# Performance work log

Hardware: AMD Instinct MI355X
Metric: run time of the kernel (lower is better)

Reference implementation:

```python
import jax, jax.numpy as jnp
import numpy as np

H, HEADS, LAYERS = 512, 4, 3
HD = H // HEADS
FFN = 4 * H
B, S = 4, 2048
EPS = 1e-5
SCALE_BASE = 512.0
GAMMAS = (1.0 - np.exp(np.linspace(np.log(1.0 / 32.0), np.log(1.0 / 512.0), HEADS))).astype(np.float32)


def _xpos(x, downscale):
    # x: [B, heads, L, d]; standard XPOS rotary with per-dim decay scale
    L, d = x.shape[-2], x.shape[-1]
    half = d // 2
    s = (jnp.arange(half, dtype=jnp.float32) + 0.4 * d) / (1.4 * d)          # [half]
    pos = jnp.arange(L, dtype=jnp.float32)
    scale = s[None, :] ** (pos[:, None] / SCALE_BASE)                         # [L, half]
    inv_freq = 1.0 / (10000.0 ** (jnp.arange(half, dtype=jnp.float32) / half))
    ang = pos[:, None] * inv_freq[None, :]                                    # [L, half]
    if downscale:
        scale = 1.0 / scale
    sin_s = jnp.repeat(jnp.sin(ang) * scale, 2, axis=-1)                      # [L, d]
    cos_s = jnp.repeat(jnp.cos(ang) * scale, 2, axis=-1)
    x1, x2 = x[..., 0::2], x[..., 1::2]
    rot = jnp.stack([-x2, x1], axis=-1).reshape(x.shape)                      # rotate_every_two
    return x * cos_s + rot * sin_s


def _layernorm(x, w, b):
    m = x.mean(-1, keepdims=True)
    v = ((x - m) ** 2).mean(-1, keepdims=True)
    return (x - m) / jnp.sqrt(v + EPS) * w + b


def _decay_mask(L):
    n = jnp.arange(L)
    nm = n[:, None] - n[None, :]
    g = jnp.asarray(GAMMAS)                                                   # [heads]
    # D[h,n,m] = gamma_h^(n-m) for n>=m else 0
    return jnp.where((nm >= 0)[None], g[:, None, None] ** jnp.maximum(nm, 0)[None], 0.0)


def _msr(X, WQ, WK, WV, WG, WO, gnw, gnb, D):
    # X: [B,S,H]; WQ/WK/WV: [heads,H,HD]; D: [heads,S,S]
    Q = _xpos(jnp.einsum('bsh,nhd->bnsd', X, WQ), False)
    K = _xpos(jnp.einsum('bsh,nhd->bnsd', X, WK), True)
    V = jnp.einsum('bsh,nhd->bnsd', X, WV)
    A = jnp.einsum('bnsd,bntd->bnst', Q, K) * D[None]                          # decay-weighted retention
    Y = jnp.einsum('bnst,bntd->bnsd', A, V)                                    # [B,heads,S,HD]
    Y = jnp.transpose(Y, (0, 2, 1, 3))                                         # [B,S,heads,HD] (head-major concat)
    m = Y.mean(-1, keepdims=True)
    v = ((Y - m) ** 2).mean(-1, keepdims=True)
    Yn = ((Y - m) / jnp.sqrt(v + EPS)).reshape(X.shape[0], X.shape[1], H) * gnw + gnb  # GroupNorm(heads, H)
    G = X @ WG
    return (G * jax.nn.sigmoid(G) * Yn) @ WO                                   # swish gate + out proj


def setup_inputs() -> dict:
    key = jax.random.key(0)
    ks = jax.random.split(key, 10)
    rn = lambda k, shape, sc: jax.random.normal(k, shape, jnp.float32) * sc
    return {
        'X': rn(ks[0], (B, S, H), 1.0),
        'WQ': rn(ks[1], (LAYERS, HEADS, H, HD), 1.0 / H),
        'WK': rn(ks[2], (LAYERS, HEADS, H, HD), 1.0 / H),
        'WV': rn(ks[3], (LAYERS, HEADS, H, HD), 1.0 / H),
        'WG': rn(ks[4], (LAYERS, H, H), 1.0 / H),
        'WO': rn(ks[5], (LAYERS, H, H), 1.0 / H),
        'gn_w': jnp.ones((LAYERS, H), jnp.float32),
        'gn_b': jnp.zeros((LAYERS, H), jnp.float32),
        'ln1_w': jnp.ones((LAYERS, H), jnp.float32),
        'ln1_b': jnp.zeros((LAYERS, H), jnp.float32),
        'ln2_w': jnp.ones((LAYERS, H), jnp.float32),
        'ln2_b': jnp.zeros((LAYERS, H), jnp.float32),
        'ffn_w1': rn(ks[6], (LAYERS, H, FFN), (2.0 / (H + FFN)) ** 0.5),
        'ffn_b1': jnp.zeros((LAYERS, FFN), jnp.float32),
        'ffn_w2': rn(ks[7], (LAYERS, FFN, H), (2.0 / (H + FFN)) ** 0.5),
        'ffn_b2': jnp.zeros((LAYERS, H), jnp.float32),
    }


def reference(X, WQ, WK, WV, WG, WO, gn_w, gn_b, ln1_w, ln1_b, ln2_w, ln2_b, ffn_w1, ffn_b1, ffn_w2, ffn_b2):
    D = _decay_mask(X.shape[1])
    for l in range(LAYERS):
        Y = _msr(_layernorm(X, ln1_w[l], ln1_b[l]), WQ[l], WK[l], WV[l], WG[l], WO[l], gn_w[l], gn_b[l], D) + X
        Hn = _layernorm(Y, ln2_w[l], ln2_b[l])
        X = jax.nn.gelu(Hn @ ffn_w1[l] + ffn_b1[l], approximate=False) @ ffn_w2[l] + ffn_b2[l] + Y
    return X, jnp.einsum('bsh,bth->bst', X, X)
```

## Files before the change

### kernel.cpp

```cpp
#include <hip/hip_runtime.h>
#include <math.h>

#define HH 512
#define NHEADS 4
#define HD 128
#define HALF 64
#define FFND 2048
#define BB 4
#define SS 2048
#define NLAYERS 3
#define ROWS (BB*SS)
#define EPSF 1e-5f
#define QKVGW 2048

typedef float f32x4 __attribute__((ext_vector_type(4)));
typedef float f32x16 __attribute__((ext_vector_type(16)));
typedef __bf16 bf16x8 __attribute__((ext_vector_type(8)));
typedef unsigned u32x2 __attribute__((ext_vector_type(2)));

__device__ __forceinline__ unsigned short f2bf(float f) {
    union { float f; unsigned u; } v; v.f = f;
    unsigned r = (v.u + 0x7FFFu + ((v.u >> 16) & 1u)) >> 16;
    return (unsigned short)r;
}
__device__ __forceinline__ float bf2f(unsigned short h) {
    union { unsigned u; float f; } v; v.u = ((unsigned)h) << 16;
    return v.f;
}
__device__ __forceinline__ void gl16(const void* g, void* l) {
    __builtin_amdgcn_global_load_lds((const __attribute__((address_space(1))) void*)g,
                                     (__attribute__((address_space(3))) void*)l, 16, 0, 0);
}
__device__ __forceinline__ bf16x8 ld8(const void* p) { return *(const bf16x8*)p; }
__device__ __forceinline__ unsigned laddr(void* p) {
    return (unsigned)(size_t)(__attribute__((address_space(3))) char*)p;
}
__device__ __forceinline__ u32x2 tr8(unsigned a) {
    u32x2 r;
    asm volatile("ds_read_b64_tr_b16 %0, %1" : "=v"(r) : "v"(a));
    return r;
}

__global__ void k_tables(float* __restrict__ cq, float* __restrict__ sq,
                         float* __restrict__ ck, float* __restrict__ sk) {
    int i = threadIdx.x;
    int s = blockIdx.x;
    float si   = ((float)i + 0.4f * (float)HD) / (1.4f * (float)HD);
    float scale = powf(si, (float)s / 512.0f);
    float invf = powf(10000.0f, -((float)i) / (float)HALF);
    float ang  = (float)s * invf;
    float c = cosf(ang), sn = sinf(ang);
    int idx = s * HALF + i;
    cq[idx] = c * scale;   sq[idx] = sn * scale;
    float is = 1.0f / scale;
    ck[idx] = c * is;      sk[idx] = sn * is;
}

__global__ __launch_bounds__(256) void k_wt(const float* __restrict__ src, unsigned short* __restrict__ dst,
                                            int K, int N, int zn, size_t sL, size_t sZ) {
    __shared__ float T[32][33];
    int n0 = blockIdx.x * 32, k0 = blockIdx.y * 32;
    int z = blockIdx.z;
    src += (size_t)z * (size_t)K * N;
    dst += (size_t)(z / zn) * sL + (size_t)(z % zn) * sZ;
    int tx = threadIdx.x & 31, ty = threadIdx.x >> 5;
    #pragma unroll
    for (int i = 0; i < 4; ++i) {
        int r = ty + i * 8;
        T[r][tx] = src[(size_t)(k0 + r) * N + n0 + tx];
    }
    __syncthreads();
    #pragma unroll
    for (int i = 0; i < 4; ++i) {
        int r = ty + i * 8;
        dst[(size_t)(n0 + r) * K + k0 + tx] = f2bf(T[tx][r]);
    }
}

__global__ __launch_bounds__(256) void k_ln(const float* __restrict__ x, const float* __restrict__ w,
                                            const float* __restrict__ b, unsigned short* __restrict__ y) {
    int lane = threadIdx.x & 63;
    size_t row = (size_t)blockIdx.x * 4 + (threadIdx.x >> 6);
    const float4* xr = (const float4*)(x + row * HH);
    float4 v0 = xr[lane * 2];
    float4 v1 = xr[lane * 2 + 1];
    float s  = v0.x + v0.y + v0.z + v0.w + v1.x + v1.y + v1.z + v1.w;
    float ss = v0.x*v0.x + v0.y*v0.y + v0.z*v0.z + v0.w*v0.w
             + v1.x*v1.x + v1.y*v1.y + v1.z*v1.z + v1.w*v1.w;
    for (int off = 32; off > 0; off >>= 1) {
        s  += __shfl_xor(s, off);
        ss += __shfl_xor(ss, off);
    }
    float m   = s * (1.0f / HH);
    float var = ss * (1.0f / HH) - m * m;
    float inv = rsqrtf(var + EPSF);
    int h0 = lane * 8;
    float4 wa = *(const float4*)(w + h0);
    float4 wb = *(const float4*)(w + h0 + 4);
    float4 ba = *(const float4*)(b + h0);
    float4 bb2 = *(const float4*)(b + h0 + 4);
    uint4 pk;
    pk.x = f2bf((v0.x - m) * inv * wa.x + ba.x) | ((unsigned)f2bf((v0.y - m) * inv * wa.y + ba.y) << 16);
    pk.y = f2bf((v0.z - m) * inv * wa.z + ba.z) | ((unsigned)f2bf((v0.w - m) * inv * wa.w + ba.w) << 16);
    pk.z = f2bf((v1.x - m) * inv * wb.x + bb2.x) | ((unsigned)f2bf((v1.y - m) * inv * wb.y + bb2.y) << 16);
    pk.w = f2bf((v1.z - m) * inv * wb.z + bb2.z) | ((unsigned)f2bf((v1.w - m) * inv * wb.w + bb2.w) << 16);
    *(uint4*)(y + row * HH + h0) = pk;
}

__global__ __launch_bounds__(256) void k_xpos(unsigned short* __restrict__ QG,
    const float* __restrict__ cq, const float* __restrict__ sq,
    const float* __restrict__ ck, const float* __restrict__ sk) {
    int row = blockIdx.x, p = threadIdx.x;
    int s = row & (SS - 1), n = p >> 6, i = p & 63;
    int ti = s * HALF + i;
    size_t qo = (size_t)row * QKVGW + n * HD + i * 2;
    unsigned qv = *(unsigned*)(QG + qo);
    float x1 = bf2f(qv & 0xffff), x2 = bf2f(qv >> 16);
    float c = cq[ti], sn = sq[ti];
    *(unsigned*)(QG + qo) = (unsigned)f2bf(x1 * c - x2 * sn) | ((unsigned)f2bf(x2 * c + x1 * sn) << 16);
    size_t ko = qo + 512;
    unsigned kv = *(unsigned*)(QG + ko);
    x1 = bf2f(kv & 0xffff); x2 = bf2f(kv >> 16);
    c = ck[ti]; sn = sk[ti];
    *(unsigned*)(QG + ko) = (unsigned)f2bf(x1 * c - x2 * sn) | ((unsigned)f2bf(x2 * c + x1 * sn) << 16);
}

__global__ __launch_bounds__(128, 2) void k_ret(
    const unsigned short* __restrict__ QG, float* __restrict__ Y) {
    __shared__ __align__(16) char sm[40960];
    const int tid = threadIdx.x;
    const int lane = tid & 63, wv = tid >> 6;
    const int l31 = lane & 31, g2 = lane >> 5;
    const int b4 = (lane >> 4) & 1;
    const int bx = blockIdx.x;
    int xs, c0;
    if (bx < 32)      { xs = 24 + (bx >> 2); c0 = bx & 3; }
    else if (bx < 56) { int i = bx - 32; int d = i / 3; xs = 16 + d; c0 = i - d * 3; }
    else if (bx < 72) { int i = bx - 56; xs = 8 + (i >> 1); c0 = i & 1; }
    else              { xs = bx - 72; c0 = 0; }
    const int hn = blockIdx.y, b = blockIdx.z;
    const int s0 = xs * 64;
    const int tstart = c0 * 8;
    const int tend = min(xs + 1, tstart + 8);
    const double la = -3.4657359027997265, lb = -6.238324625039508;
    const float gamma = (float)(1.0 - exp(la + (lb - la) * ((double)hn / 3.0)));
    const float l2g = log2f(gamma);
    const size_t rowbase = (size_t)b * SS;
    const int qcol = hn * HD, kcol = 512 + hn * HD, vcol = 1024 + hn * HD;
    const char* Gp = (const char*)QG;

    const int srow = s0 + wv * 32 + l31;
    bf16x8 qf[8];
    #pragma unroll
    for (int kc = 0; kc < 8; ++kc)
        qf[kc] = ld8(QG + (rowbase + srow) * QKVGW + qcol + kc * 16 + g2 * 8);

    float gq[4], gj[4];
    #pragma unroll
    for (int q = 0; q < 4; ++q) { gq[q] = exp2f(-l2g * (8.0f * q)); gj[q] = exp2f(-l2g * (float)q); }
    const float gt32m = exp2f(-l2g * 32.0f);

    f32x16 accy[4];
    #pragma unroll
    for (int d = 0; d < 4; ++d)
        #pragma unroll
        for (int e = 0; e < 16; ++e) accy[d][e] = 0.0f;

    const int sloc = wv * 32 + l31;
    const int ssw = (sloc & 7) << 4;
    const int r15 = (l31 & 15) << 4;
    const unsigned vbase = laddr(sm + 16384) + b4 * 2048 + g2 * 256 + (lane & 15) * 2;

    for (int t = tstart; t < tend; ++t) {
        const int t0 = t * 64;
        __syncthreads();
        #pragma unroll
        for (int c = 0; c < 8; ++c) {
            int chunk = wv * 8 + c;
            int r = chunk * 4 + (lane >> 4);
            int w = ((lane & 15) * 16) ^ ((r & 15) << 4);
            gl16(Gp + ((rowbase + t0 + r) * QKVGW + kcol) * 2 + w, sm + chunk * 1024);
        }
        #pragma unroll
        for (int c = 0; c < 8; ++c) {
            int chunk = wv * 8 + c;
            int slot = chunk * 64 + lane;
            int sub = slot >> 3, w8 = slot & 7;
            int db = sub >> 4, tb = sub & 15;
            int tl = tb * 4 + (w8 >> 1);
            int d  = db * 16 + (w8 & 1) * 8;
            gl16(Gp + ((rowbase + t0 + tl) * QKVGW + vcol + d) * 2, sm + 16384 + chunk * 1024);
        }
        __syncthreads();
        f32x16 pacc0, pacc1;
        #pragma unroll
        for (int e = 0; e < 16; ++e) { pacc0[e] = 0.0f; pacc1[e] = 0.0f; }
        #pragma unroll
        for (int kc = 0; kc < 8; ++kc) {
            bf16x8 k0 = ld8(sm + l31 * 256 + ((kc * 32 + g2 * 16) ^ r15));
            bf16x8 k1 = ld8(sm + (32 + l31) * 256 + ((kc * 32 + g2 * 16) ^ r15));
            pacc0 = __builtin_amdgcn_mfma_f32_32x32x16_bf16(k0, qf[kc], pacc0, 0, 0, 0);
            pacc1 = __builtin_amdgcn_mfma_f32_32x32x16_bf16(k1, qf[kc], pacc1, 0, 0, 0);
        }
        const float G0 = exp2f(l2g * (float)(srow - t0 - g2 * 4));
        #pragma unroll
        for (int tb2 = 0; tb2 < 2; ++tb2) {
            const float gb = tb2 ? gt32m : 1.0f;
            #pragma unroll
            for (int q = 0; q < 4; ++q) {
                unsigned short u0, u1, u2, u3;
                int tbase = t0 + tb2 * 32 + q * 8 + g2 * 4;
                float base = G0 * gb * gq[q];
                float p0 = (tb2 ? pacc1 : pacc0)[q * 4 + 0];
                float p1 = (tb2 ? pacc1 : pacc0)[q * 4 + 1];
                float p2 = (tb2 ? pacc1 : pacc0)[q * 4 + 2];
                float p3 = (tb2 ? pacc1 : pacc0)[q * 4 + 3];
                u0 = f2bf((srow >= tbase + 0) ? p0 * base * gj[0] : 0.0f);
                u1 = f2bf((srow >= tbase + 1) ? p1 * base * gj[1] : 0.0f);
                u2 = f2bf((srow >= tbase + 2) ? p2 * base * gj[2] : 0.0f);
                u3 = f2bf((srow >= tbase + 3) ? p3 * base * gj[3] : 0.0f);
                u32x2 pk2;
                pk2.x = (unsigned)u0 | ((unsigned)u1 << 16);
                pk2.y = (unsigned)u2 | ((unsigned)u3 << 16);
                *(u32x2*)(sm + 32768 + ((sloc * 128 + tb2 * 64 + q * 16 + g2 * 8) ^ ssw)) = pk2;
            }
        }
        bf16x8 pf[4];
        #pragma unroll
        for (int tc = 0; tc < 4; ++tc)
            pf[tc] = ld8(sm + 32768 + ((sloc * 128 + tc * 32 + g2 * 16) ^ ssw));
        #pragma unroll
        for (int dblk = 0; dblk < 4; ++dblk) {
            u32x2 va[4], vb[4];
            #pragma unroll
            for (int tc = 0; tc < 4; ++tc) {
                unsigned a0 = vbase + dblk * 4096 + tc * 512;
                va[tc] = tr8(a0);
                vb[tc] = tr8(a0 + 128);
            }
            asm volatile("s_waitcnt lgkmcnt(0)" ::: "memory");
            __builtin_amdgcn_sched_barrier(0);
            #pragma unroll
            for (int tc = 0; tc < 4; ++tc) {
                union { u32x2 u[2]; bf16x8 v; } cvt;
                cvt.u[0] = va[tc]; cvt.u[1] = vb[tc];
                accy[dblk] = __builtin_amdgcn_mfma_f32_32x32x16_bf16(pf[tc], cvt.v, accy[dblk], 0, 0, 0);
            }
        }
    }
    if (xs < 8) {
        #pragma unroll
        for (int dblk = 0; dblk < 4; ++dblk)
            #pragma unroll
            for (int rg = 0; rg < 16; ++rg) {
                int sl2 = s0 + wv * 32 + (rg & 3) + (rg >> 2) * 8 + g2 * 4;
                Y[(rowbase + sl2) * HH + hn * HD + dblk * 32 + l31] = accy[dblk][rg];
            }
    } else {
        #pragma unroll
        for (int dblk = 0; dblk < 4; ++dblk)
            #pragma unroll
            for (int rg = 0; rg < 16; ++rg) {
                int sl2 = s0 + wv * 32 + (rg & 3) + (rg >> 2) * 8 + g2 * 4;
                unsafeAtomicAdd(&Y[(rowbase + sl2) * HH + hn * HD + dblk * 32 + l31], accy[dblk][rg]);
            }
    }
}

__global__ __launch_bounds__(256) void k_gate(
    const float* __restrict__ Yr, const unsigned short* __restrict__ QG,
    const float* __restrict__ gw, const float* __restrict__ gb,
    unsigned short* __restrict__ E) {
    int lane = threadIdx.x & 63;
    int grp  = blockIdx.x * 4 + (threadIdx.x >> 6);
    int row = grp >> 2, nh = grp & 3;
    size_t off = (size_t)row * HH + nh * HD + lane * 2;
    float2 v = *(const float2*)(Yr + off);
    float s = v.x + v.y, ss = v.x * v.x + v.y * v.y;
    for (int o = 32; o > 0; o >>= 1) {
        s  += __shfl_xor(s, o);
        ss += __shfl_xor(ss, o);
    }
    float m   = s * (1.0f / HD);
    float var = ss * (1.0f / HD) - m * m;
    float inv = rsqrtf(var + EPSF);
    int h = nh * HD + lane * 2;
    unsigned gv = *(const unsigned*)(QG + (size_t)row * QKVGW + 1536 + nh * HD + lane * 2);
    float g0 = bf2f(gv & 0xffff), g1 = bf2f(gv >> 16);
    float2 w2 = *(const float2*)(gw + h), b2 = *(const float2*)(gb + h);
    float yn0 = (v.x - m) * inv * w2.x + b2.x;
    float yn1 = (v.y - m) * inv * w2.y + b2.y;
    float e0v = g0 / (1.0f + expf(-g0)) * yn0;
    float e1v = g1 / (1.0f + expf(-g1)) * yn1;
    *(unsigned*)(E + off) = (unsigned)f2bf(e0v) | ((unsigned)f2bf(e1v) << 16);
}

template<int EPI, int OUTBF>
__global__ __launch_bounds__(256) void k_mm(
    const unsigned short* __restrict__ A, const unsigned short* __restrict__ Bt,
    void* __restrict__ Cv, const float* __restrict__ bias, const float* __restrict__ Rs,
    int M, int N, int K, size_t aB, size_t bB, size_t cB,
    unsigned short* __restrict__ C2) {
    __shared__ __align__(16) char sm[16384];
    const int tid = threadIdx.x;
    const int lane = tid & 63, wid = tid >> 6;
    const int wr = wid >> 1, wc = wid & 1;
    const int lcol = lane & 15, lrow = lane >> 4;
    const size_t m0 = (size_t)blockIdx.x * 128, n0 = (size_t)blockIdx.y * 128;
    const char* Ab = (const char*)(A + (size_t)blockIdx.z * aB);
    const char* Bb = (const char*)(Bt + (size_t)blockIdx.z * bB);
    f32x4 acc[4][4];
    #pragma unroll
    for (int i = 0; i < 4; ++i)
        #pragma unroll
        for (int j = 0; j < 4; ++j) acc[i][j] = f32x4{0.f, 0.f, 0.f, 0.f};
    for (int k0 = 0; k0 < K; k0 += 32) {
        __syncthreads();
        #pragma unroll
        for (int c = 0; c < 2; ++c) {
            int chunk = wid * 2 + c;
            int r = chunk * 16 + (lane >> 2);
            int w = ((lane & 3) ^ (r & 3)) << 4;
            gl16(Ab + ((size_t)(m0 + r) * K + k0) * 2 + w, sm + chunk * 1024);
            gl16(Bb + ((size_t)(n0 + r) * K + k0) * 2 + w, sm + 8192 + chunk * 1024);
        }
        __syncthreads();
        bf16x8 af[4], bfr[4];
        #pragma unroll
        for (int m = 0; m < 4; ++m) {
            int r = wr * 64 + m * 16 + lcol;
            af[m] = ld8(sm + r * 64 + ((lrow * 16) ^ ((r & 3) << 4)));
        }
        #pragma unroll
        for (int n2 = 0; n2 < 4; ++n2) {
            int r = wc * 64 + n2 * 16 + lcol;
            bfr[n2] = ld8(sm + 8192 + r * 64 + ((lrow * 16) ^ ((r & 3) << 4)));
        }
        #pragma unroll
        for (int m = 0; m < 4; ++m)
            #pragma unroll
            for (int n2 = 0; n2 < 4; ++n2)
                acc[m][n2] = __builtin_amdgcn_mfma_f32_16x16x32_bf16(af[m], bfr[n2], acc[m][n2], 0, 0, 0);
    }
    float* Cf = (float*)Cv + (size_t)blockIdx.z * cB;
    unsigned short* Cb = (unsigned short*)Cv + (size_t)blockIdx.z * cB;
    const float* Rb = (EPI >= 2) ? (Rs + (size_t)blockIdx.z * cB) : nullptr;
    #pragma unroll
    for (int m = 0; m < 4; ++m) {
        #pragma unroll
        for (int n2 = 0; n2 < 4; ++n2) {
            size_t col = n0 + wc * 64 + n2 * 16 + lcol;
            float bc = (EPI == 1 || EPI == 2 || EPI == 4) ? bias[col] : 0.0f;
            #pragma unroll
            for (int j = 0; j < 4; ++j) {
                size_t row = m0 + wr * 64 + m * 16 + lrow * 4 + j;
                float v = acc[m][n2][j];
                if (EPI == 1) { v += bc; v = 0.5f * v * (1.0f + erff(v * 0.70710678118654752f)); }
                else if (EPI == 2 || EPI == 4) v += bc + Rb[row * N + col];
                else if (EPI == 3) v += Rb[row * N + col];
                if (EPI == 4) {
                    Cf[row * N + col] = v;
                    C2[row * N + col] = f2bf(v);
                } else if (OUTBF) Cb[row * N + col] = f2bf(v);
                else              Cf[row * N + col] = v;
            }
        }
    }
}

extern "C" void kernel_launch(void* const* d_in, const int* in_sizes, int n_in,
                              void* d_out, int out_size, void* d_ws, size_t ws_size,
                              hipStream_t stream) {
    const float* X0  = (const float*)d_in[0];
    const float* WQ  = (const float*)d_in[1];
    const float* WK  = (const float*)d_in[2];
    const float* WV  = (const float*)d_in[3];
    const float* WG  = (const float*)d_in[4];
    const float* WO  = (const float*)d_in[5];
    const float* gnw = (const float*)d_in[6];
    const float* gnb = (const float*)d_in[7];
    const float* l1w = (const float*)d_in[8];
    const float* l1b = (const float*)d_in[9];
    const float* l2w = (const float*)d_in[10];
    const float* l2b = (const float*)d_in[11];
    const float* fw1 = (const float*)d_in[12];
    const float* fb1 = (const float*)d_in[13];
    const float* fw2 = (const float*)d_in[14];
    const float* fb2 = (const float*)d_in[15];
    float* outX = (float*)d_out;
    float* outG = outX + (size_t)ROWS * HH;

    char* wp = (char*)d_ws;
    auto take = [&](size_t bytes) { char* p = wp; wp += (bytes + 255) & ~(size_t)255; return p; };
    float* cq = (float*)take((size_t)SS * HALF * 4);
    float* sq = (float*)take((size_t)SS * HALF * 4);
    float* ck = (float*)take((size_t)SS * HALF * 4);
    float* sk = (float*)take((size_t)SS * HALF * 4);
    unsigned short* Wcat = (unsigned short*)take((size_t)NLAYERS * QKVGW * HH * 2);
    unsigned short* WOt = (unsigned short*)take((size_t)NLAYERS * HH * HH * 2);
    unsigned short* F1t = (unsigned short*)take((size_t)NLAYERS * HH * FFND * 2);
    unsigned short* F2t = (unsigned short*)take((size_t)NLAYERS * HH * FFND * 2);
    unsigned short* Xn  = (unsigned short*)take((size_t)ROWS * HH * 2);
    unsigned short* QKVG = (unsigned short*)take((size_t)ROWS * QKVGW * 2);
    unsigned short* Eb  = (unsigned short*)take((size_t)ROWS * HH * 2);
    float* Yr   = (float*)take((size_t)ROWS * HH * 4);
    float* Y2   = (float*)take((size_t)ROWS * HH * 4);
    float* Xbuf = (float*)take((size_t)ROWS * HH * 4);
    unsigned short* Hb = (unsigned short*)take((size_t)ROWS * FFND * 2);
    unsigned short* Xb = Xn;

    k_tables<<<SS, HALF, 0, stream>>>(cq, sq, ck, sk);
    k_wt<<<dim3(4, 16, 12), 256, 0, stream>>>(WQ, Wcat, HH, HD, 4, (size_t)QKVGW * HH, (size_t)HD * HH);
    k_wt<<<dim3(4, 16, 12), 256, 0, stream>>>(WK, Wcat + (size_t)512 * HH, HH, HD, 4, (size_t)QKVGW * HH, (size_t)HD * HH);
    k_wt<<<dim3(4, 16, 12), 256, 0, stream>>>(WV, Wcat + (size_t)1024 * HH, HH, HD, 4, (size_t)QKVGW * HH, (size_t)HD * HH);
    k_wt<<<dim3(16, 16, 3), 256, 0, stream>>>(WG, Wcat + (size_t)1536 * HH, HH, HH, 1, (size_t)QKVGW * HH, 0);
    k_wt<<<dim3(16, 16, 3), 256, 0, stream>>>(WO, WOt, HH, HH, 1, (size_t)HH * HH, 0);
    k_wt<<<dim3(64, 16, 3), 256, 0, stream>>>(fw1, F1t, HH, FFND, 1, (size_t)HH * FFND, 0);
    k_wt<<<dim3(16, 64, 3), 256, 0, stream>>>(fw2, F2t, FFND, HH, 1, (size_t)FFND * HH, 0);

    const float* curX = X0;
    for (int l = 0; l < NLAYERS; ++l) {
        const unsigned short* Bc = Wcat + (size_t)l * QKVGW * HH;
        const unsigned short* Bo = WOt + (size_t)l * HH * HH;
        const unsigned short* B1 = F1t + (size_t)l * HH * FFND;
        const unsigned short* B2 = F2t + (size_t)l * HH * FFND;
        k_ln<<<ROWS / 4, 256, 0, stream>>>(curX, l1w + l * HH, l1b + l * HH, Xn);
        dim3 gq(ROWS / 128, QKVGW / 128, 1);
        k_mm<0, 1><<<gq, 256, 0, stream>>>(Xn, Bc, QKVG, nullptr, nullptr, ROWS, QKVGW, HH, 0, 0, 0, nullptr);
        k_xpos<<<ROWS, 256, 0, stream>>>(QKVG, cq, sq, ck, sk);
        hipMemsetAsync(Yr, 0, (size_t)ROWS * HH * 4, stream);
        k_ret<<<dim3(80, NHEADS, BB), 128, 0, stream>>>(QKVG, Yr);
        k_gate<<<ROWS, 256, 0, stream>>>(Yr, QKVG, gnw + l * HH, gnb + l * HH, Eb);
        dim3 g1(ROWS / 128, HH / 128, 1);
        k_mm<3, 0><<<g1, 256, 0, stream>>>(Eb, Bo, Y2, nullptr, curX, ROWS, HH, HH, 0, 0, 0, nullptr);
        k_ln<<<ROWS / 4, 256, 0, stream>>>(Y2, l2w + l * HH, l2b + l * HH, Xn);
        dim3 g2(ROWS / 128, FFND / 128, 1);
        k_mm<1, 1><<<g2, 256, 0, stream>>>(Xn, B1, Hb, fb1 + (size_t)l * FFND, nullptr, ROWS, FFND, HH, 0, 0, 0, nullptr);
        if (l == NLAYERS - 1) {
            k_mm<4, 0><<<g1, 256, 0, stream>>>(Hb, B2, outX, fb2 + (size_t)l * HH, Y2, ROWS, HH, FFND, 0, 0, 0, Xb);
        } else {
            k_mm<2, 0><<<g1, 256, 0, stream>>>(Hb, B2, Xbuf, fb2 + (size_t)l * HH, Y2, ROWS, HH, FFND, 0, 0, 0, nullptr);
        }
        curX = Xbuf;
    }
    dim3 g3(SS / 128, SS / 128, BB);
    k_mm<0, 0><<<g3, 256, 0, stream>>>(Xb, Xb, outG, nullptr, nullptr, SS, SS, HH,
                                       (size_t)SS * HH, (size_t)SS * HH, (size_t)SS * SS, nullptr);
}
```

Measured before the change: 893.1 us.

## Double-buffer K/V staging in retention kernel with 128-row query tiles

The retention kernel now uses 256-thread blocks covering 128 query rows, with a rebuilt triangular work split across 40 blocks per head and batch. K/V tiles are prefetched into a second LDS buffer while the current tile is computed, using vmcnt waits and raw barriers in place of the two syncthreads per iteration. The full memset of the output is replaced by a small kernel that zeroes only the rows later filled by atomics. LDS use doubles to 80 KB per block, which limits occupancy, and the longer per-block chunks may change load balance.

```diff
diff --git a/kernel.cpp b/kernel.cpp
--- a/kernel.cpp
+++ b/kernel.cpp
@@ -125,23 +125,32 @@
     *(unsigned*)(QG + ko) = (unsigned)f2bf(x1 * c - x2 * sn) | ((unsigned)f2bf(x2 * c + x1 * sn) << 16);
 }
 
-__global__ __launch_bounds__(128, 2) void k_ret(
+__global__ __launch_bounds__(256) void k_zero(float* __restrict__ Y) {
+    int idx = blockIdx.x * 256 + threadIdx.x;
+    int bb = idx / 196608;
+    int rem = idx - bb * 196608;
+    float4 zz = {0.f, 0.f, 0.f, 0.f};
+    *(float4*)(Y + (size_t)bb * (SS * HH) + (size_t)512 * HH + (size_t)rem * 4) = zz;
+}
+
+__global__ __launch_bounds__(256, 2) void k_ret(
     const unsigned short* __restrict__ QG, float* __restrict__ Y) {
-    __shared__ __align__(16) char sm[40960];
+    __shared__ __align__(16) char sm[81920];
     const int tid = threadIdx.x;
     const int lane = tid & 63, wv = tid >> 6;
     const int l31 = lane & 31, g2 = lane >> 5;
     const int b4 = (lane >> 4) & 1;
     const int bx = blockIdx.x;
-    int xs, c0;
-    if (bx < 32)      { xs = 24 + (bx >> 2); c0 = bx & 3; }
-    else if (bx < 56) { int i = bx - 32; int d = i / 3; xs = 16 + d; c0 = i - d * 3; }
-    else if (bx < 72) { int i = bx - 56; xs = 8 + (i >> 1); c0 = i & 1; }
-    else              { xs = bx - 72; c0 = 0; }
+    int xs, c0 = 0;
+    if (bx < 16)      { xs = 15 - (bx >> 2); c0 = bx & 3; }
+    else if (bx < 28) { int i = bx - 16; xs = 11 - i / 3; c0 = i % 3; }
+    else if (bx < 36) { int i = bx - 28; xs = 7 - (i >> 1); c0 = i & 1; }
+    else              { xs = 39 - bx; }
     const int hn = blockIdx.y, b = blockIdx.z;
-    const int s0 = xs * 64;
+    const int s0 = xs * 128;
+    const int nt = 2 * xs + 2;
     const int tstart = c0 * 8;
-    const int tend = min(xs + 1, tstart + 8);
+    const int tend = min(nt, tstart + 8);
     const double la = -3.4657359027997265, lb = -6.238324625039508;
     const float gamma = (float)(1.0 - exp(la + (lb - la) * ((double)hn / 3.0)));
     const float l2g = log2f(gamma);
@@ -169,86 +178,104 @@
     const int sloc = wv * 32 + l31;
     const int ssw = (sloc & 7) << 4;
     const int r15 = (l31 & 15) << 4;
-    const unsigned vbase = laddr(sm + 16384) + b4 * 2048 + g2 * 256 + (lane & 15) * 2;
-
-    for (int t = tstart; t < tend; ++t) {
-        const int t0 = t * 64;
-        __syncthreads();
-        #pragma unroll
-        for (int c = 0; c < 8; ++c) {
-            int chunk = wv * 8 + c;
+
+    auto stage = [&](int t0, int buf) {
+        #pragma unroll
+        for (int c = 0; c < 4; ++c) {
+            int chunk = wv * 4 + c;
             int r = chunk * 4 + (lane >> 4);
             int w = ((lane & 15) * 16) ^ ((r & 15) << 4);
-            gl16(Gp + ((rowbase + t0 + r) * QKVGW + kcol) * 2 + w, sm + chunk * 1024);
-        }
-        #pragma unroll
-        for (int c = 0; c < 8; ++c) {
-            int chunk = wv * 8 + c;
+            gl16(Gp + ((rowbase + t0 + r) * QKVGW + kcol) * 2 + w, sm + buf * 16384 + chunk * 1024);
+        }
+        #pragma unroll
+        for (int c = 0; c < 4; ++c) {
+            int chunk = wv * 4 + c;
             int slot = chunk * 64 + lane;
             int sub = slot >> 3, w8 = slot & 7;
             int db = sub >> 4, tb = sub & 15;
             int tl = tb * 4 + (w8 >> 1);
             int d  = db * 16 + (w8 & 1) * 8;
-            gl16(Gp + ((rowbase + t0 + tl) * QKVGW + vcol + d) * 2, sm + 16384 + chunk * 1024);
-        }
-        __syncthreads();
-        f32x16 pacc0, pacc1;
-        #pragma unroll
-        for (int e = 0; e < 16; ++e) { pacc0[e] = 0.0f; pacc1[e] = 0.0f; }
-        #pragma unroll
-        for (int kc = 0; kc < 8; ++kc) {
-            bf16x8 k0 = ld8(sm + l31 * 256 + ((kc * 32 + g2 * 16) ^ r15));
-            bf16x8 k1 = ld8(sm + (32 + l31) * 256 + ((kc * 32 + g2 * 16) ^ r15));
-            pacc0 = __builtin_amdgcn_mfma_f32_32x32x16_bf16(k0, qf[kc], pacc0, 0, 0, 0);
-            pacc1 = __builtin_amdgcn_mfma_f32_32x32x16_bf16(k1, qf[kc], pacc1, 0, 0, 0);
-        }
-        const float G0 = exp2f(l2g * (float)(srow - t0 - g2 * 4));
-        #pragma unroll
-        for (int tb2 = 0; tb2 < 2; ++tb2) {
-            const float gb = tb2 ? gt32m : 1.0f;
-            #pragma unroll
-            for (int q = 0; q < 4; ++q) {
-                unsigned short u0, u1, u2, u3;
-                int tbase = t0 + tb2 * 32 + q * 8 + g2 * 4;
-                float base = G0 * gb * gq[q];
-                float p0 = (tb2 ? pacc1 : pacc0)[q * 4 + 0];
-                float p1 = (tb2 ? pacc1 : pacc0)[q * 4 + 1];
-                float p2 = (tb2 ? pacc1 : pacc0)[q * 4 + 2];
-                float p3 = (tb2 ? pacc1 : pacc0)[q * 4 + 3];
-                u0 = f2bf((srow >= tbase + 0) ? p0 * base * gj[0] : 0.0f);
-                u1 = f2bf((srow >= tbase + 1) ? p1 * base * gj[1] : 0.0f);
-                u2 = f2bf((srow >= tbase + 2) ? p2 * base * gj[2] : 0.0f);
-                u3 = f2bf((srow >= tbase + 3) ? p3 * base * gj[3] : 0.0f);
-                u32x2 pk2;
-                pk2.x = (unsigned)u0 | ((unsigned)u1 << 16);
-                pk2.y = (unsigned)u2 | ((unsigned)u3 << 16);
-                *(u32x2*)(sm + 32768 + ((sloc * 128 + tb2 * 64 + q * 16 + g2 * 8) ^ ssw)) = pk2;
-            }
-        }
-        bf16x8 pf[4];
-        #pragma unroll
-        for (int tc = 0; tc < 4; ++tc)
-            pf[tc] = ld8(sm + 32768 + ((sloc * 128 + tc * 32 + g2 * 16) ^ ssw));
-        #pragma unroll
-        for (int dblk = 0; dblk < 4; ++dblk) {
-            u32x2 va[4], vb[4];
-            #pragma unroll
-            for (int tc = 0; tc < 4; ++tc) {
-                unsigned a0 = vbase + dblk * 4096 + tc * 512;
-                va[tc] = tr8(a0);
-                vb[tc] = tr8(a0 + 128);
-            }
-            asm volatile("s_waitcnt lgkmcnt(0)" ::: "memory");
-            __builtin_amdgcn_sched_barrier(0);
-            #pragma unroll
-            for (int tc = 0; tc < 4; ++tc) {
-                union { u32x2 u[2]; bf16x8 v; } cvt;
-                cvt.u[0] = va[tc]; cvt.u[1] = vb[tc];
-                accy[dblk] = __builtin_amdgcn_mfma_f32_32x32x16_bf16(pf[tc], cvt.v, accy[dblk], 0, 0, 0);
-            }
-        }
-    }
-    if (xs < 8) {
+            gl16(Gp + ((rowbase + t0 + tl) * QKVGW + vcol + d) * 2, sm + 32768 + buf * 16384 + chunk * 1024);
+        }
+    };
+
+    int cur = 0;
+    stage(tstart * 64, 0);
+    for (int t = tstart; t < tend; ++t) {
+        const int t0 = t * 64;
+        if (t + 1 < tend) {
+            stage((t + 1) * 64, cur ^ 1);
+            asm volatile("s_waitcnt vmcnt(8)" ::: "memory");
+        } else {
+            asm volatile("s_waitcnt vmcnt(0)" ::: "memory");
+        }
+        __builtin_amdgcn_sched_barrier(0);
+        __builtin_amdgcn_s_barrier();
+        __builtin_amdgcn_sched_barrier(0);
+        {
+            const char* kb = sm + cur * 16384;
+            f32x16 pacc0, pacc1;
+            #pragma unroll
+            for (int e = 0; e < 16; ++e) { pacc0[e] = 0.0f; pacc1[e] = 0.0f; }
+            #pragma unroll
+            for (int kc = 0; kc < 8; ++kc) {
+                bf16x8 k0 = ld8(kb + l31 * 256 + ((kc * 32 + g2 * 16) ^ r15));
+                bf16x8 k1 = ld8(kb + (32 + l31) * 256 + ((kc * 32 + g2 * 16) ^ r15));
+                pacc0 = __builtin_amdgcn_mfma_f32_32x32x16_bf16(k0, qf[kc], pacc0, 0, 0, 0);
+                pacc1 = __builtin_amdgcn_mfma_f32_32x32x16_bf16(k1, qf[kc], pacc1, 0, 0, 0);
+            }
+            const float G0 = exp2f(l2g * (float)(srow - t0 - g2 * 4));
+            #pragma unroll
+            for (int tb2 = 0; tb2 < 2; ++tb2) {
+                const float gb = tb2 ? gt32m : 1.0f;
+                #pragma unroll
+                for (int q = 0; q < 4; ++q) {
+                    int tbase = t0 + tb2 * 32 + q * 8 + g2 * 4;
+                    float base = G0 * gb * gq[q];
+                    float p0 = (tb2 ? pacc1 : pacc0)[q * 4 + 0];
+                    float p1 = (tb2 ? pacc1 : pacc0)[q * 4 + 1];
+                    float p2 = (tb2 ? pacc1 : pacc0)[q * 4 + 2];
+                    float p3 = (tb2 ? pacc1 : pacc0)[q * 4 + 3];
+                    unsigned short u0 = f2bf((srow >= tbase + 0) ? p0 * base * gj[0] : 0.0f);
+                    unsigned short u1 = f2bf((srow >= tbase + 1) ? p1 * base * gj[1] : 0.0f);
+                    unsigned short u2 = f2bf((srow >= tbase + 2) ? p2 * base * gj[2] : 0.0f);
+                    unsigned short u3 = f2bf((srow >= tbase + 3) ? p3 * base * gj[3] : 0.0f);
+                    u32x2 pk2;
+                    pk2.x = (unsigned)u0 | ((unsigned)u1 << 16);
+                    pk2.y = (unsigned)u2 | ((unsigned)u3 << 16);
+                    *(u32x2*)(sm + 65536 + ((sloc * 128 + tb2 * 64 + q * 16 + g2 * 8) ^ ssw)) = pk2;
+                }
+            }
+            bf16x8 pf[4];
+            #pragma unroll
+            for (int tc = 0; tc < 4; ++tc)
+                pf[tc] = ld8(sm + 65536 + ((sloc * 128 + tc * 32 + g2 * 16) ^ ssw));
+            const unsigned vbase = laddr(sm + 32768 + cur * 16384) + b4 * 2048 + g2 * 256 + (lane & 15) * 2;
+            #pragma unroll
+            for (int dblk = 0; dblk < 4; ++dblk) {
+                u32x2 va[4], vb[4];
+                #pragma unroll
+                for (int tc = 0; tc < 4; ++tc) {
+                    unsigned a0 = vbase + dblk * 4096 + tc * 512;
+                    va[tc] = tr8(a0);
+                    vb[tc] = tr8(a0 + 128);
+                }
+                asm volatile("s_waitcnt lgkmcnt(0)" ::: "memory");
+                __builtin_amdgcn_sched_barrier(0);
+                #pragma unroll
+                for (int tc = 0; tc < 4; ++tc) {
+                    union { u32x2 u[2]; bf16x8 v; } cvt;
+                    cvt.u[0] = va[tc]; cvt.u[1] = vb[tc];
+                    accy[dblk] = __builtin_amdgcn_mfma_f32_32x32x16_bf16(pf[tc], cvt.v, accy[dblk], 0, 0, 0);
+                }
+            }
+        }
+        __builtin_amdgcn_sched_barrier(0);
+        __builtin_amdgcn_s_barrier();
+        __builtin_amdgcn_sched_barrier(0);
+        cur ^= 1;
+    }
+    if (xs < 4) {
         #pragma unroll
         for (int dblk = 0; dblk < 4; ++dblk)
             #pragma unroll
@@ -428,8 +455,8 @@
         dim3 gq(ROWS / 128, QKVGW / 128, 1);
         k_mm<0, 1><<<gq, 256, 0, stream>>>(Xn, Bc, QKVG, nullptr, nullptr, ROWS, QKVGW, HH, 0, 0, 0, nullptr);
         k_xpos<<<ROWS, 256, 0, stream>>>(QKVG, cq, sq, ck, sk);
-        hipMemsetAsync(Yr, 0, (size_t)ROWS * HH * 4, stream);
-        k_ret<<<dim3(80, NHEADS, BB), 128, 0, stream>>>(QKVG, Yr);
+        k_zero<<<3072, 256, 0, stream>>>(Yr);
+        k_ret<<<dim3(40, NHEADS, BB), 256, 0, stream>>>(QKVG, Yr);
         k_gate<<<ROWS, 256, 0, stream>>>(Yr, QKVG, gnw + l * HH, gnb + l * HH, Eb);
         dim3 g1(ROWS / 128, HH / 128, 1);
         k_mm<3, 0><<<g1, 256, 0, stream>>>(Eb, Bo, Y2, nullptr, curX, ROWS, HH, HH, 0, 0, 0, nullptr);
```

After: 870.5 us. -2.5%, faster.
